# Optimization experiments

Measured on AMD Instinct MI355X. Metric: run time of the kernel, lower is better.

Reference implementation:

```python
import jax, jax.numpy as jnp
import numpy as np

B, S, D, H, BS, L, FF, V = 2, 4096, 1024, 16, 64, 4, 4096, 50000
HD = D // H; NB = S // BS; NM = NB - 2; R = 3

def layernorm(x, g, b):
    mu = x.mean(-1, keepdims=True)
    var = ((x - mu) ** 2).mean(-1, keepdims=True)
    return (x - mu) * jax.lax.rsqrt(var + 1e-5) * g + b

def bigbird_attn(x, neg, rand_attn, Wq, bq, Wk, bk, Wv, bv, Wo, bo):
    heads = lambda t: t.reshape(B, S, H, HD).transpose(0, 2, 1, 3)
    q, k, v = heads(x @ Wq + bq), heads(x @ Wk + bk), heads(x @ Wv + bv)
    scale = np.float32(1.0 / np.sqrt(HD))
    qb = q.reshape(B, H, NB, BS, HD); kb = k.reshape(B, H, NB, BS, HD); vb = v.reshape(B, H, NB, BS, HD)
    negb = neg.reshape(B, NB, BS)
    # global query blocks (first & last) attend densely to all keys
    qg = jnp.concatenate([qb[:, :, 0], qb[:, :, -1]], axis=2)  # [B,H,2*BS,HD]
    sg = jnp.einsum('bhqd,bhkd->bhqk', qg, k) * scale + neg[:, None, None, :]
    ctx_g = jnp.einsum('bhqk,bhkd->bhqd', jax.nn.softmax(sg, -1), v)
    # middle query blocks: sliding window(3) + global(2) + random(R) key blocks
    win_k = jnp.stack([kb[:, :, i:i + NM] for i in range(3)], axis=3)  # [B,H,NM,3,BS,HD]
    win_v = jnp.stack([vb[:, :, i:i + NM] for i in range(3)], axis=3)
    gidx = jnp.array([0, NB - 1])
    g_k = jnp.broadcast_to(kb[:, :, gidx][:, :, None], (B, H, NM, 2, BS, HD))
    g_v = jnp.broadcast_to(vb[:, :, gidx][:, :, None], (B, H, NM, 2, BS, HD))
    hix = jnp.arange(H)[:, None, None]
    r_k = kb[:, hix, rand_attn]  # [B,H,NM,R,BS,HD]
    r_v = vb[:, hix, rand_attn]
    K = 3 + 2 + R
    keys = jnp.concatenate([win_k, g_k, r_k], axis=3).reshape(B, H, NM, K * BS, HD)
    vals = jnp.concatenate([win_v, g_v, r_v], axis=3).reshape(B, H, NM, K * BS, HD)
    win_m = jnp.stack([negb[:, i:i + NM] for i in range(3)], axis=2)  # [B,NM,3,BS]
    g_m = jnp.broadcast_to(negb[:, gidx][:, None], (B, NM, 2, BS))
    m_wg = jnp.concatenate([win_m, g_m], axis=2).reshape(B, 1, NM, 5 * BS)
    r_m = negb[:, rand_attn].reshape(B, H, NM, R * BS)
    m_all = jnp.concatenate([jnp.broadcast_to(m_wg, (B, H, NM, 5 * BS)), r_m], axis=-1)
    sm = jnp.einsum('bhnqd,bhnkd->bhnqk', qb[:, :, 1:-1], keys) * scale + m_all[:, :, :, None, :]
    ctx_m = jnp.einsum('bhnqk,bhnkd->bhnqd', jax.nn.softmax(sm, -1), vals)
    ctx = jnp.concatenate([ctx_g[:, :, None, :BS], ctx_m, ctx_g[:, :, None, BS:]], axis=2)
    out = ctx.reshape(B, H, S, HD).transpose(0, 2, 1, 3).reshape(B, S, D)
    return out @ Wo + bo

def reference(input_ids, attention_mask, rand_attn, emb, Wq, bq, Wk, bk, Wv, bv, Wo, bo, ln1_g, ln1_b, W1, b1, W2, b2, ln2_g, ln2_b, lnf_g, lnf_b, projW, projb):
    x = emb[input_ids]
    neg = (1.0 - attention_mask.astype(jnp.float32)) * (-1e9)
    for l in range(L):  # pre-norm transformer encoder layers
        x = x + bigbird_attn(layernorm(x, ln1_g[l], ln1_b[l]), neg, rand_attn,
                             Wq[l], bq[l], Wk[l], bk[l], Wv[l], bv[l], Wo[l], bo[l])
        h = layernorm(x, ln2_g[l], ln2_b[l])
        x = x + (jax.nn.gelu(h @ W1[l] + b1[l]) @ W2[l] + b2[l])
    x = layernorm(x, lnf_g, lnf_b)
    feats = x.mean(axis=1)  # pooled output (mean over tokens)
    feats = feats / jnp.maximum(jnp.linalg.norm(feats, axis=-1, keepdims=True), 1e-12)
    return feats @ projW + projb

def setup_inputs():
    key = jax.random.key(0)
    ks = jax.random.split(key, 16)
    init = lambda k, shp: (0.02 * jax.random.normal(k, shp)).astype(jnp.float32)
    return {
        'input_ids': jax.random.randint(ks[0], (B, S), 0, V),
        'attention_mask': jnp.ones((B, S), dtype=jnp.int32),
        'rand_attn': jax.random.randint(ks[1], (H, NM, R), 1, NB - 1),
        'emb': init(ks[2], (V, D)),
        'Wq': init(ks[3], (L, D, D)), 'bq': jnp.zeros((L, D), jnp.float32),
        'Wk': init(ks[4], (L, D, D)), 'bk': jnp.zeros((L, D), jnp.float32),
        'Wv': init(ks[5], (L, D, D)), 'bv': jnp.zeros((L, D), jnp.float32),
        'Wo': init(ks[6], (L, D, D)), 'bo': jnp.zeros((L, D), jnp.float32),
        'ln1_g': jnp.ones((L, D), jnp.float32), 'ln1_b': jnp.zeros((L, D), jnp.float32),
        'W1': init(ks[7], (L, D, FF)), 'b1': jnp.zeros((L, FF), jnp.float32),
        'W2': init(ks[8], (L, FF, D)), 'b2': jnp.zeros((L, D), jnp.float32),
        'ln2_g': jnp.ones((L, D), jnp.float32), 'ln2_b': jnp.zeros((L, D), jnp.float32),
        'lnf_g': jnp.ones((D,), jnp.float32), 'lnf_b': jnp.zeros((D,), jnp.float32),
        'projW': init(ks[9], (D, 512)), 'projb': jnp.zeros((512,), jnp.float32),
    }
```

## Files before the change

### kernel.cpp

```cpp
#include <hip/hip_runtime.h>
#include <hip/hip_bf16.h>
#include <cstdint>
#include <cstddef>

#define BATCH 2
#define SEQ   4096
#define DIM   1024
#define NHEAD 16
#define HDIM  64
#define NBLK  64
#define NMID  62
#define NRAND 3
#define NLAYER 4
#define FFDIM 4096
#define ROWS  (BATCH*SEQ)
#define KSPL  8

using f32x4 = __attribute__((ext_vector_type(4))) float;
using s16x8 = __attribute__((ext_vector_type(8))) short;
using s16x4 = __attribute__((ext_vector_type(4))) short;

__device__ inline float bf2f(short s) {
    unsigned u = ((unsigned)(unsigned short)s) << 16;
    union { unsigned u; float f; } cv; cv.u = u; return cv.f;
}
__device__ inline short f2bf(float f) {
    union { float f; unsigned u; } cv; cv.f = f;
    unsigned u = cv.u;
    unsigned r = (u + 0x7fffu + ((u >> 16) & 1u)) >> 16;
    return (short)r;
}
__device__ inline float gelu_f(float x) {
    float u = 0.7978845608028654f * (x + 0.044715f * x * x * x);
    return 0.5f * x * (1.f + tanhf(u));
}

__global__ __launch_bounds__(256) void embed_kernel(
    const int* __restrict__ ids, const float* __restrict__ emb, float* __restrict__ x)
{
    int row = blockIdx.x;
    int id  = ids[row];
    ((float4*)x)[(size_t)row * 256 + threadIdx.x] =
        ((const float4*)emb)[(size_t)id * 256 + threadIdx.x];
}

__global__ __launch_bounds__(256) void neg_kernel(
    const int* __restrict__ mask, float* __restrict__ neg)
{
    int i = blockIdx.x * 256 + threadIdx.x;
    if (i < ROWS) neg[i] = (1.f - (float)mask[i]) * -1e9f;
}

template<int OUTBF>
__global__ __launch_bounds__(256) void ln_kernel(
    const float* __restrict__ x, const float* __restrict__ g,
    const float* __restrict__ bia, void* __restrict__ out)
{
    __shared__ float s1[4], s2[4];
    int row = blockIdx.x, t = threadIdx.x;
    const float* xr = x + (size_t)row * DIM;
    float4 v = ((const float4*)xr)[t];
    float s = v.x + v.y + v.z + v.w;
    #pragma unroll
    for (int o = 32; o > 0; o >>= 1) s += __shfl_xor(s, o, 64);
    if ((t & 63) == 0) s1[t >> 6] = s;
    __syncthreads();
    float mu = (s1[0] + s1[1] + s1[2] + s1[3]) * (1.f / DIM);
    float dx = v.x - mu, dy = v.y - mu, dz = v.z - mu, dw = v.w - mu;
    float q = dx*dx + dy*dy + dz*dz + dw*dw;
    #pragma unroll
    for (int o = 32; o > 0; o >>= 1) q += __shfl_xor(q, o, 64);
    if ((t & 63) == 0) s2[t >> 6] = q;
    __syncthreads();
    float var = (s2[0] + s2[1] + s2[2] + s2[3]) * (1.f / DIM);
    float rs  = rsqrtf(var + 1e-5f);
    float4 gg = ((const float4*)g)[t];
    float4 bb = ((const float4*)bia)[t];
    float o0 = dx * rs * gg.x + bb.x;
    float o1 = dy * rs * gg.y + bb.y;
    float o2 = dz * rs * gg.z + bb.z;
    float o3 = dw * rs * gg.w + bb.w;
    if (OUTBF) {
        s16x4 ov = { f2bf(o0), f2bf(o1), f2bf(o2), f2bf(o3) };
        ((s16x4*)out)[(size_t)row * (DIM/4) + t] = ov;
    } else {
        float4 ov = { o0, o1, o2, o3 };
        ((float4*)out)[(size_t)row * (DIM/4) + t] = ov;
    }
}

__global__ __launch_bounds__(256) void wconv_kernel(
    const float* __restrict__ W, short* __restrict__ Wt, int K, int N)
{
    __shared__ float tile[32][33];
    int k0 = blockIdx.x * 32, n0 = blockIdx.y * 32;
    int t = threadIdx.x;
    int r = t >> 3, c = (t & 7) * 4;
    float4 v = *(const float4*)(W + (size_t)(k0 + r) * N + n0 + c);
    tile[r][c+0] = v.x; tile[r][c+1] = v.y; tile[r][c+2] = v.z; tile[r][c+3] = v.w;
    __syncthreads();
    s16x4 ov;
    #pragma unroll
    for (int jj = 0; jj < 4; ++jj) ov[jj] = f2bf(tile[c + jj][r]);
    *(s16x4*)(Wt + (size_t)(n0 + r) * K + k0 + c) = ov;
}

__global__ __launch_bounds__(256) void vtrans_kernel(
    const short* __restrict__ vbuf, short* __restrict__ vT)
{
    __shared__ short tile[64][66];
    const int sb = blockIdx.x, h = blockIdx.y, b = blockIdx.z;
    const int t = threadIdx.x;
    {
        int row = t >> 2, c0 = (t & 3) * 16;
        const short* src = vbuf + (size_t)(b * SEQ + sb * 64 + row) * DIM + h * HDIM + c0;
        s16x8 a0 = ((const s16x8*)src)[0];
        s16x8 a1 = ((const s16x8*)src)[1];
        #pragma unroll
        for (int i = 0; i < 8; ++i) { tile[row][c0 + i] = a0[i]; tile[row][c0 + 8 + i] = a1[i]; }
    }
    __syncthreads();
    {
        int d = t >> 2, k0 = (t & 3) * 16;
        s16x8 o0, o1;
        #pragma unroll
        for (int i = 0; i < 8; ++i) { o0[i] = tile[k0 + i][d]; o1[i] = tile[k0 + 8 + i][d]; }
        short* dst = vT + (size_t)((b * NHEAD + h) * HDIM + d) * SEQ + sb * 64 + k0;
        ((s16x8*)dst)[0] = o0;
        ((s16x8*)dst)[1] = o1;
    }
}

template<int EPI>
__global__ __launch_bounds__(256) void gemm_kernel(
    const short* __restrict__ A, const short* __restrict__ Bt,
    const float* __restrict__ bias, const float* __restrict__ resid,
    void* __restrict__ Cout, int M, int N, int K)
{
    __shared__ short As[128 * 64];
    __shared__ short Bs[128 * 64];
    const int t = threadIdx.x;
    const int m0 = blockIdx.x * 128, n0 = blockIdx.y * 128;
    const int lane = t & 63, wave = t >> 6;
    const int wr = (wave >> 1) * 64, wc = (wave & 1) * 64;
    const int srow = t >> 3;
    const int scolb = (t & 7) * 16;

    f32x4 acc[4][4];
    #pragma unroll
    for (int m = 0; m < 4; ++m)
        #pragma unroll
        for (int n = 0; n < 4; ++n)
            acc[m][n] = f32x4{0.f, 0.f, 0.f, 0.f};

    const short* Arow = A  + (size_t)(m0 + srow) * K + (scolb >> 1);
    const short* Brow = Bt + (size_t)(n0 + srow) * K + (scolb >> 1);

    for (int kt = 0; kt < K; kt += 64) {
        s16x8 ra[4], rb[4];
        #pragma unroll
        for (int p = 0; p < 4; ++p) {
            ra[p] = *(const s16x8*)(Arow + (size_t)(p * 32) * K + kt);
            rb[p] = *(const s16x8*)(Brow + (size_t)(p * 32) * K + kt);
        }
        __syncthreads();
        #pragma unroll
        for (int p = 0; p < 4; ++p) {
            int row = p * 32 + srow;
            int boff = row * 128 + (scolb ^ ((row & 7) << 4));
            *(s16x8*)((char*)As + boff) = ra[p];
            *(s16x8*)((char*)Bs + boff) = rb[p];
        }
        __syncthreads();
        #pragma unroll
        for (int kk = 0; kk < 2; ++kk) {
            s16x8 af[4], bfr[4];
            #pragma unroll
            for (int i = 0; i < 4; ++i) {
                int cb = kk * 64 + ((lane >> 4) << 4);
                int r  = wr + i * 16 + (lane & 15);
                af[i]  = *(const s16x8*)((const char*)As + r * 128 + (cb ^ ((r & 7) << 4)));
                int r2 = wc + i * 16 + (lane & 15);
                bfr[i] = *(const s16x8*)((const char*)Bs + r2 * 128 + (cb ^ ((r2 & 7) << 4)));
            }
            #pragma unroll
            for (int m = 0; m < 4; ++m)
                #pragma unroll
                for (int n = 0; n < 4; ++n)
                    acc[m][n] = __builtin_amdgcn_mfma_f32_16x16x32_bf16(
                        af[m], bfr[n], acc[m][n], 0, 0, 0);
        }
    }

    const int rbase = m0 + wr + ((lane >> 4) << 2);
    const int cbase = n0 + wc + (lane & 15);
    #pragma unroll
    for (int m = 0; m < 4; ++m) {
        #pragma unroll
        for (int n = 0; n < 4; ++n) {
            #pragma unroll
            for (int j = 0; j < 4; ++j) {
                int row = rbase + m * 16 + j;
                int col = cbase + n * 16;
                float val = acc[m][n][j] + bias[col];
                size_t idx = (size_t)row * N + col;
                if (EPI == 1) val = gelu_f(val);
                if (EPI == 2) ((float*)Cout)[idx] = val + resid[idx];
                else          ((short*)Cout)[idx] = f2bf(val);
            }
        }
    }
}


__device__ inline void attn_tile_mfma(
    const short* __restrict__ kglob,
    const short* __restrict__ vtglob,
    const float* __restrict__ negp,
    short* Ks, short* Vs, float* kmask,
    const s16x8* qfrag, f32x4* o, float& mr, float& lsum)
{
    const int t = threadIdx.x;
    const int lane = t & 63;
    const int q15 = lane & 15, g = lane >> 4;
    const int sw = (lane & 7) << 4;

    {
        int row = t >> 2, c0 = (t & 3) * 16;
        int rsw = (row & 7) << 4;
        const short* ksrc = kglob + (size_t)row * DIM + c0;
        s16x8 a0 = ((const s16x8*)ksrc)[0];
        s16x8 a1 = ((const s16x8*)ksrc)[1];
        char* kdst = (char*)Ks + row * 128;
        *(s16x8*)(kdst + ((c0 * 2)      ^ rsw)) = a0;
        *(s16x8*)(kdst + ((c0 * 2 + 16) ^ rsw)) = a1;
        const short* vsrc = vtglob + (size_t)row * SEQ + c0;
        s16x8 b0 = ((const s16x8*)vsrc)[0];
        s16x8 b1 = ((const s16x8*)vsrc)[1];
        char* vdst = (char*)Vs + row * 128;
        *(s16x8*)(vdst + ((c0 * 2)      ^ rsw)) = b0;
        *(s16x8*)(vdst + ((c0 * 2 + 16) ^ rsw)) = b1;
        if (t < 16) ((float4*)kmask)[t] = ((const float4*)negp)[t];
    }
    __syncthreads();

    f32x4 s[4];
    #pragma unroll
    for (int f = 0; f < 4; ++f) s[f] = f32x4{0.f, 0.f, 0.f, 0.f};
    #pragma unroll
    for (int ch = 0; ch < 2; ++ch) {
        #pragma unroll
        for (int f = 0; f < 4; ++f) {
            s16x8 kf = *(const s16x8*)((const char*)Ks + (16 * f + q15) * 128 + ((ch * 64 + g * 16) ^ sw));
            s[f] = __builtin_amdgcn_mfma_f32_16x16x32_bf16(kf, qfrag[ch], s[f], 0, 0, 0);
        }
    }

    float p[4][4];
    float mt = -1e30f;
    #pragma unroll
    for (int f = 0; f < 4; ++f) {
        float4 km = ((const float4*)kmask)[f * 4 + g];
        #pragma unroll
        for (int j = 0; j < 4; ++j) {
            float val = s[f][j] * 0.125f + ((const float*)&km)[j];
            p[f][j] = val;
            mt = fmaxf(mt, val);
        }
    }
    mt = fmaxf(mt, __shfl_xor(mt, 16, 64));
    mt = fmaxf(mt, __shfl_xor(mt, 32, 64));
    float mn = fmaxf(mr, mt);
    float psum = 0.f;
    #pragma unroll
    for (int f = 0; f < 4; ++f)
        #pragma unroll
        for (int j = 0; j < 4; ++j) {
            float e = __expf(p[f][j] - mn);
            p[f][j] = e;
            psum += e;
        }
    psum += __shfl_xor(psum, 16, 64);
    psum += __shfl_xor(psum, 32, 64);
    float fc = __expf(mr - mn);
    mr = mn;
    lsum = lsum * fc + psum;
    #pragma unroll
    for (int dt = 0; dt < 4; ++dt)
        #pragma unroll
        for (int j = 0; j < 4; ++j) o[dt][j] *= fc;

    unsigned pk[4][2];
    #pragma unroll
    for (int f = 0; f < 4; ++f)
        #pragma unroll
        for (int pp = 0; pp < 2; ++pp)
            pk[f][pp] = ((unsigned)(unsigned short)f2bf(p[f][2 * pp + 1]) << 16)
                      |  (unsigned)(unsigned short)f2bf(p[f][2 * pp]);

    const int bsel = (lane >> 4) & 1, asel = (lane >> 5) & 1;
    #pragma unroll
    for (int c = 0; c < 2; ++c) {
        union { s16x8 v; int u[4]; } pb;
        #pragma unroll
        for (int w = 0; w < 4; ++w) {
            int src = q15 + 16 * (2 * bsel + (w >> 1));
            int lo = __shfl((int)pk[2 * c][w & 1], src, 64);
            int hi = __shfl((int)pk[2 * c + 1][w & 1], src, 64);
            pb.u[w] = asel ? hi : lo;
        }
        #pragma unroll
        for (int dt = 0; dt < 4; ++dt) {
            s16x8 vf = *(const s16x8*)((const char*)Vs + (16 * dt + q15) * 128 + ((c * 64 + g * 16) ^ sw));
            o[dt] = __builtin_amdgcn_mfma_f32_16x16x32_bf16(vf, pb.v, o[dt], 0, 0, 0);
        }
    }
    __syncthreads();
}

__device__ inline void stage_q64_swz(const short* __restrict__ qglob, short* Qs)
{
    int t = threadIdx.x;
    int row = t >> 2, c0 = (t & 3) * 16;
    int rsw = (row & 7) << 4;
    const short* src = qglob + (size_t)row * DIM + c0;
    s16x8 a0 = ((const s16x8*)src)[0];
    s16x8 a1 = ((const s16x8*)src)[1];
    char* dst = (char*)Qs + row * 128;
    *(s16x8*)(dst + ((c0 * 2)      ^ rsw)) = a0;
    *(s16x8*)(dst + ((c0 * 2 + 16) ^ rsw)) = a1;
}

__global__ __launch_bounds__(256) void attn_middle_mfma(
    const short* __restrict__ q, const short* __restrict__ k, const short* __restrict__ vT,
    const float* __restrict__ neg, const int* __restrict__ rand_attn, short* __restrict__ ctx)
{
    __shared__ short Qs[64 * 64];
    __shared__ short Ks[64 * 64];
    __shared__ short Vs[64 * 64];
    __shared__ float kmask[64];

    const int j = blockIdx.x, h = blockIdx.y, b = blockIdx.z;
    const int n = j + 1;
    const int t = threadIdx.x;
    const int lane = t & 63, wave = t >> 6;
    const int q15 = lane & 15, g = lane >> 4;
    const int sw = (lane & 7) << 4;

    stage_q64_swz(q + (size_t)(b * SEQ + n * 64) * DIM + h * HDIM, Qs);
    __syncthreads();

    s16x8 qfrag[2];
    {
        int qrow = wave * 16 + q15;
        #pragma unroll
        for (int ch = 0; ch < 2; ++ch)
            qfrag[ch] = *(const s16x8*)((const char*)Qs + qrow * 128 + ((ch * 64 + g * 16) ^ sw));
    }

    int kbl[8];
    kbl[0] = n - 1; kbl[1] = n; kbl[2] = n + 1; kbl[3] = 0; kbl[4] = NBLK - 1;
    {
        const int* ra = rand_attn + ((size_t)h * NMID + j) * NRAND;
        kbl[5] = ra[0]; kbl[6] = ra[1]; kbl[7] = ra[2];
    }

    f32x4 o[4];
    #pragma unroll
    for (int dt = 0; dt < 4; ++dt) o[dt] = f32x4{0.f, 0.f, 0.f, 0.f};
    float mr = -1e30f, lsum = 0.f;

    const short* kbase  = k  + (size_t)b * SEQ * DIM + h * HDIM;
    const short* vtbase = vT + (size_t)(b * NHEAD + h) * HDIM * SEQ;
    const float* negb   = neg + (size_t)b * SEQ;

    #pragma unroll 1
    for (int ib = 0; ib < 8; ++ib) {
        int kbn = kbl[ib];
        attn_tile_mfma(kbase + (size_t)kbn * 64 * DIM, vtbase + kbn * 64,
                       negb + kbn * 64, Ks, Vs, kmask, qfrag, o, mr, lsum);
    }

    float inv = 1.f / lsum;
    short* obase = ctx + (size_t)(b * SEQ + n * 64 + wave * 16 + q15) * DIM + h * HDIM;
    #pragma unroll
    for (int dt = 0; dt < 4; ++dt) {
        s16x4 ov;
        #pragma unroll
        for (int jj = 0; jj < 4; ++jj) ov[jj] = f2bf(o[dt][jj] * inv);
        *(s16x4*)(obase + dt * 16 + g * 4) = ov;
    }
}

__global__ __launch_bounds__(256) void attn_global_mfma(
    const short* __restrict__ q, const short* __restrict__ k, const short* __restrict__ vT,
    const float* __restrict__ neg, float* __restrict__ part)
{
    __shared__ short Qs[64 * 64];
    __shared__ short Ks[64 * 64];
    __shared__ short Vs[64 * 64];
    __shared__ float kmask[64];

    const int qb = blockIdx.x >> 3, ks = blockIdx.x & 7;
    const int h = blockIdx.y, b = blockIdx.z;
    const int tok0 = qb ? (SEQ - 64) : 0;
    const int t = threadIdx.x;
    const int lane = t & 63, wave = t >> 6;
    const int q15 = lane & 15, g = lane >> 4;
    const int sw = (lane & 7) << 4;

    stage_q64_swz(q + (size_t)(b * SEQ + tok0) * DIM + h * HDIM, Qs);
    __syncthreads();

    s16x8 qfrag[2];
    {
        int qrow = wave * 16 + q15;
        #pragma unroll
        for (int ch = 0; ch < 2; ++ch)
            qfrag[ch] = *(const s16x8*)((const char*)Qs + qrow * 128 + ((ch * 64 + g * 16) ^ sw));
    }

    f32x4 o[4];
    #pragma unroll
    for (int dt = 0; dt < 4; ++dt) o[dt] = f32x4{0.f, 0.f, 0.f, 0.f};
    float mr = -1e30f, lsum = 0.f;

    const short* kbase  = k  + (size_t)b * SEQ * DIM + h * HDIM;
    const short* vtbase = vT + (size_t)(b * NHEAD + h) * HDIM * SEQ;
    const float* negb   = neg + (size_t)b * SEQ;

    #pragma unroll 1
    for (int ib = 0; ib < 8; ++ib) {
        int kbn = ks * 8 + ib;
        attn_tile_mfma(kbase + (size_t)kbn * 64 * DIM, vtbase + kbn * 64,
                       negb + kbn * 64, Ks, Vs, kmask, qfrag, o, mr, lsum);
    }

    float* pbase = part + ((size_t)(((b * NHEAD + h) * 2 + qb) * KSPL + ks)) * 4224;
    int qrow = wave * 16 + q15;
    #pragma unroll
    for (int dt = 0; dt < 4; ++dt)
        *(f32x4*)(pbase + qrow * 64 + dt * 16 + g * 4) = o[dt];
    if (g == 0) { pbase[4096 + qrow] = mr; pbase[4160 + qrow] = lsum; }
}

__global__ __launch_bounds__(256) void attn_greduce(
    const float* __restrict__ part, short* __restrict__ ctx)
{
    const int qb = blockIdx.x, h = blockIdx.y, b = blockIdx.z;
    const int tok0 = qb ? (SEQ - 64) : 0;
    const int t = threadIdx.x;
    const int qq = t >> 2, d0 = (t & 3) * 16;
    const float* base = part + ((size_t)(((b * NHEAD + h) * 2 + qb) * KSPL)) * 4224;

    float m = -1e30f;
    #pragma unroll 1
    for (int s = 0; s < KSPL; ++s)
        m = fmaxf(m, base[(size_t)s * 4224 + 4096 + qq]);
    float L = 0.f;
    float acc[16];
    #pragma unroll
    for (int i = 0; i < 16; ++i) acc[i] = 0.f;
    #pragma unroll 1
    for (int s = 0; s < KSPL; ++s) {
        const float* bp = base + (size_t)s * 4224;
        float w = __expf(bp[4096 + qq] - m);
        L += w * bp[4160 + qq];
        const float4* row = (const float4*)(bp + qq * 64 + d0);
        #pragma unroll
        for (int v4 = 0; v4 < 4; ++v4) {
            float4 val = row[v4];
            acc[v4 * 4 + 0] = fmaf(w, val.x, acc[v4 * 4 + 0]);
            acc[v4 * 4 + 1] = fmaf(w, val.y, acc[v4 * 4 + 1]);
            acc[v4 * 4 + 2] = fmaf(w, val.z, acc[v4 * 4 + 2]);
            acc[v4 * 4 + 3] = fmaf(w, val.w, acc[v4 * 4 + 3]);
        }
    }
    float inv = 1.f / L;
    short* dst = ctx + (size_t)(b * SEQ + tok0 + qq) * DIM + h * HDIM + d0;
    s16x8 o0, o1;
    #pragma unroll
    for (int i = 0; i < 8; ++i) { o0[i] = f2bf(acc[i] * inv); o1[i] = f2bf(acc[8 + i] * inv); }
    ((s16x8*)dst)[0] = o0;
    ((s16x8*)dst)[1] = o1;
}

__global__ __launch_bounds__(256) void colmean_kernel(
    const float* __restrict__ xln, float* __restrict__ feats)
{
    __shared__ float red[8][33];
    int c = blockIdx.x, b = blockIdx.y;
    int dd = threadIdx.x & 31, rg = threadIdx.x >> 5;
    const float* base = xln + (size_t)b * SEQ * DIM + c * 32 + dd;
    float s = 0.f;
    for (int rr = rg; rr < SEQ; rr += 8) s += base[(size_t)rr * DIM];
    red[rg][dd] = s;
    __syncthreads();
    if (rg == 0) {
        float tot = s;
        #pragma unroll
        for (int i = 1; i < 8; ++i) tot += red[i][dd];
        feats[b * DIM + c * 32 + dd] = tot * (1.f / SEQ);
    }
}

__global__ __launch_bounds__(256) void head_kernel(
    const float* __restrict__ feats, const float* __restrict__ projW,
    const float* __restrict__ projb, float* __restrict__ out)
{
    __shared__ float f[DIM];
    __shared__ float slots[4];
    int b = blockIdx.x, t = threadIdx.x;
    float ss = 0.f;
    for (int i = t; i < DIM; i += 256) {
        float vv = feats[b * DIM + i];
        f[i] = vv;
        ss += vv * vv;
    }
    #pragma unroll
    for (int o = 32; o > 0; o >>= 1) ss += __shfl_xor(ss, o, 64);
    if ((t & 63) == 0) slots[t >> 6] = ss;
    __syncthreads();
    float nrm = sqrtf(slots[0] + slots[1] + slots[2] + slots[3]);
    float inv = 1.f / fmaxf(nrm, 1e-12f);
    for (int o = t; o < 512; o += 256) {
        float acc = 0.f;
        for (int d = 0; d < DIM; ++d)
            acc = fmaf(f[d], projW[(size_t)d * 512 + o], acc);
        out[b * 512 + o] = acc * inv + projb[o];
    }
}

extern "C" void kernel_launch(void* const* d_in, const int* in_sizes, int n_in,
                              void* d_out, int out_size, void* d_ws, size_t ws_size,
                              hipStream_t stream)
{
    (void)in_sizes; (void)n_in; (void)out_size; (void)ws_size;
    const int*   ids   = (const int*)d_in[0];
    const int*   amask = (const int*)d_in[1];
    const int*   rnd   = (const int*)d_in[2];
    const float* emb   = (const float*)d_in[3];
    const float* Wq    = (const float*)d_in[4];
    const float* bq    = (const float*)d_in[5];
    const float* Wk    = (const float*)d_in[6];
    const float* bk    = (const float*)d_in[7];
    const float* Wv    = (const float*)d_in[8];
    const float* bv    = (const float*)d_in[9];
    const float* Wo    = (const float*)d_in[10];
    const float* bo    = (const float*)d_in[11];
    const float* ln1g  = (const float*)d_in[12];
    const float* ln1b  = (const float*)d_in[13];
    const float* W1    = (const float*)d_in[14];
    const float* b1    = (const float*)d_in[15];
    const float* W2    = (const float*)d_in[16];
    const float* b2    = (const float*)d_in[17];
    const float* ln2g  = (const float*)d_in[18];
    const float* ln2b  = (const float*)d_in[19];
    const float* lnfg  = (const float*)d_in[20];
    const float* lnfb  = (const float*)d_in[21];
    const float* projW = (const float*)d_in[22];
    const float* projb = (const float*)d_in[23];
    float* out = (float*)d_out;

    char* ws = (char*)d_ws;
    size_t off = 0;
    float* x    = (float*)(ws + off); off += (size_t)ROWS * DIM * 4;
    float* xn_f = (float*)(ws + off);
    short* xn_b = (short*)(ws + off); off += (size_t)ROWS * DIM * 4;
    short* qb   = (short*)(ws + off); off += (size_t)ROWS * DIM * 2;
    short* kbuf = (short*)(ws + off); off += (size_t)ROWS * DIM * 2;
    short* vbuf = (short*)(ws + off); off += (size_t)ROWS * DIM * 2;
    short* vT   = (short*)(ws + off); off += (size_t)ROWS * DIM * 2;
    short* ctxb = (short*)(ws + off); off += (size_t)ROWS * DIM * 2;
    short* ffb  = (short*)(ws + off); off += (size_t)ROWS * FFDIM * 2;
    short* wt   = (short*)(ws + off); off += (size_t)FFDIM * DIM * 2;
    float* neg  = (float*)(ws + off); off += (size_t)ROWS * 4;
    float* feats= (float*)(ws + off); off += (size_t)BATCH * DIM * 4;
    float* part = (float*)(ws + off); off += (size_t)BATCH * NHEAD * 2 * KSPL * 4224 * 4;

    embed_kernel<<<ROWS, 256, 0, stream>>>(ids, emb, x);
    neg_kernel<<<(ROWS + 255) / 256, 256, 0, stream>>>(amask, neg);

    for (int l = 0; l < NLAYER; ++l) {
        ln_kernel<1><<<ROWS, 256, 0, stream>>>(x, ln1g + l * DIM, ln1b + l * DIM, xn_b);

        wconv_kernel<<<dim3(DIM/32, DIM/32), 256, 0, stream>>>(Wq + (size_t)l*DIM*DIM, wt, DIM, DIM);
        gemm_kernel<0><<<dim3(ROWS/128, DIM/128), 256, 0, stream>>>(xn_b, wt, bq + l*DIM, nullptr, qb,   ROWS, DIM, DIM);
        wconv_kernel<<<dim3(DIM/32, DIM/32), 256, 0, stream>>>(Wk + (size_t)l*DIM*DIM, wt, DIM, DIM);
        gemm_kernel<0><<<dim3(ROWS/128, DIM/128), 256, 0, stream>>>(xn_b, wt, bk + l*DIM, nullptr, kbuf, ROWS, DIM, DIM);
        wconv_kernel<<<dim3(DIM/32, DIM/32), 256, 0, stream>>>(Wv + (size_t)l*DIM*DIM, wt, DIM, DIM);
        gemm_kernel<0><<<dim3(ROWS/128, DIM/128), 256, 0, stream>>>(xn_b, wt, bv + l*DIM, nullptr, vbuf, ROWS, DIM, DIM);

        vtrans_kernel<<<dim3(SEQ/64, NHEAD, BATCH), 256, 0, stream>>>(vbuf, vT);

        attn_global_mfma<<<dim3(2 * KSPL, NHEAD, BATCH), 256, 0, stream>>>(qb, kbuf, vT, neg, part);
        attn_middle_mfma<<<dim3(NMID, NHEAD, BATCH), 256, 0, stream>>>(qb, kbuf, vT, neg, rnd, ctxb);
        attn_greduce<<<dim3(2, NHEAD, BATCH), 256, 0, stream>>>(part, ctxb);

        wconv_kernel<<<dim3(DIM/32, DIM/32), 256, 0, stream>>>(Wo + (size_t)l*DIM*DIM, wt, DIM, DIM);
        gemm_kernel<2><<<dim3(ROWS/128, DIM/128), 256, 0, stream>>>(ctxb, wt, bo + l*DIM, x, x, ROWS, DIM, DIM);

        ln_kernel<1><<<ROWS, 256, 0, stream>>>(x, ln2g + l * DIM, ln2b + l * DIM, xn_b);

        wconv_kernel<<<dim3(DIM/32, FFDIM/32), 256, 0, stream>>>(W1 + (size_t)l*DIM*FFDIM, wt, DIM, FFDIM);
        gemm_kernel<1><<<dim3(ROWS/128, FFDIM/128), 256, 0, stream>>>(xn_b, wt, b1 + l*FFDIM, nullptr, ffb, ROWS, FFDIM, DIM);
        wconv_kernel<<<dim3(FFDIM/32, DIM/32), 256, 0, stream>>>(W2 + (size_t)l*FFDIM*DIM, wt, FFDIM, DIM);
        gemm_kernel<2><<<dim3(ROWS/128, DIM/128), 256, 0, stream>>>(ffb, wt, b2 + l*DIM, x, x, ROWS, DIM, FFDIM);
    }

    ln_kernel<0><<<ROWS, 256, 0, stream>>>(x, lnfg, lnfb, xn_f);
    colmean_kernel<<<dim3(32, BATCH), 256, 0, stream>>>(xn_f, feats);
    head_kernel<<<BATCH, 256, 0, stream>>>(feats, projW, projb, out);
}
```

Baseline: 1.972 ms.

## Fuse QKV GEMMs, use direct global-to-LDS loads, parallelize column mean

The Q, K and V projections now share one concatenated weight and bias and run as a single GEMM into an interleaved qkv buffer, and the attention kernels read it with a 3*DIM stride. The GEMM mainloop stages tiles with global_load_lds (16-byte direct-to-LDS loads), dropping the register round trip and the XOR swizzle, and adds a trailing barrier. The final column mean becomes a two-stage reduction over many more blocks. Risks: without the swizzle, LDS reads may hit bank conflicts, and the GEMM still has no double buffering.

```diff
diff --git a/kernel.cpp b/kernel.cpp
--- a/kernel.cpp
+++ b/kernel.cpp
@@ -15,6 +15,7 @@
 #define FFDIM 4096
 #define ROWS  (BATCH*SEQ)
 #define KSPL  8
+#define QKVLD (3*DIM)
 
 using f32x4 = __attribute__((ext_vector_type(4))) float;
 using s16x8 = __attribute__((ext_vector_type(8))) short;
@@ -35,6 +36,13 @@
     return 0.5f * x * (1.f + tanhf(u));
 }
 
+__device__ inline void gload16(const short* g, short* l) {
+    __builtin_amdgcn_global_load_lds(
+        (const __attribute__((address_space(1))) void*)g,
+        (__attribute__((address_space(3))) void*)l,
+        16, 0, 0);
+}
+
 __global__ __launch_bounds__(256) void embed_kernel(
     const int* __restrict__ ids, const float* __restrict__ emb, float* __restrict__ x)
 {
@@ -49,6 +57,15 @@
 {
     int i = blockIdx.x * 256 + threadIdx.x;
     if (i < ROWS) neg[i] = (1.f - (float)mask[i]) * -1e9f;
+}
+
+__global__ __launch_bounds__(256) void biaspack_kernel(
+    const float* __restrict__ bq, const float* __restrict__ bk,
+    const float* __restrict__ bv, float* __restrict__ b3)
+{
+    int i = blockIdx.x * 256 + threadIdx.x;
+    float v = (i < DIM) ? bq[i] : (i < 2 * DIM) ? bk[i - DIM] : bv[i - 2 * DIM];
+    b3[i] = v;
 }
 
 template<int OUTBF>
@@ -106,14 +123,14 @@
 }
 
 __global__ __launch_bounds__(256) void vtrans_kernel(
-    const short* __restrict__ vbuf, short* __restrict__ vT)
+    const short* __restrict__ qkv, short* __restrict__ vT)
 {
     __shared__ short tile[64][66];
     const int sb = blockIdx.x, h = blockIdx.y, b = blockIdx.z;
     const int t = threadIdx.x;
     {
         int row = t >> 2, c0 = (t & 3) * 16;
-        const short* src = vbuf + (size_t)(b * SEQ + sb * 64 + row) * DIM + h * HDIM + c0;
+        const short* src = qkv + 2 * DIM + (size_t)(b * SEQ + sb * 64 + row) * QKVLD + h * HDIM + c0;
         s16x8 a0 = ((const s16x8*)src)[0];
         s16x8 a1 = ((const s16x8*)src)[1];
         #pragma unroll
@@ -143,8 +160,8 @@
     const int m0 = blockIdx.x * 128, n0 = blockIdx.y * 128;
     const int lane = t & 63, wave = t >> 6;
     const int wr = (wave >> 1) * 64, wc = (wave & 1) * 64;
-    const int srow = t >> 3;
-    const int scolb = (t & 7) * 16;
+    const int lrow = lane >> 3;
+    const int lk   = (lane & 7) * 8;
 
     f32x4 acc[4][4];
     #pragma unroll
@@ -153,23 +170,13 @@
         for (int n = 0; n < 4; ++n)
             acc[m][n] = f32x4{0.f, 0.f, 0.f, 0.f};
 
-    const short* Arow = A  + (size_t)(m0 + srow) * K + (scolb >> 1);
-    const short* Brow = Bt + (size_t)(n0 + srow) * K + (scolb >> 1);
-
     for (int kt = 0; kt < K; kt += 64) {
-        s16x8 ra[4], rb[4];
-        #pragma unroll
-        for (int p = 0; p < 4; ++p) {
-            ra[p] = *(const s16x8*)(Arow + (size_t)(p * 32) * K + kt);
-            rb[p] = *(const s16x8*)(Brow + (size_t)(p * 32) * K + kt);
-        }
-        __syncthreads();
-        #pragma unroll
-        for (int p = 0; p < 4; ++p) {
-            int row = p * 32 + srow;
-            int boff = row * 128 + (scolb ^ ((row & 7) << 4));
-            *(s16x8*)((char*)As + boff) = ra[p];
-            *(s16x8*)((char*)Bs + boff) = rb[p];
+        #pragma unroll
+        for (int c = 0; c < 4; ++c) {
+            int chunk = wave * 4 + c;
+            int row = chunk * 8 + lrow;
+            gload16(A  + (size_t)(m0 + row) * K + kt + lk, As + chunk * 512);
+            gload16(Bt + (size_t)(n0 + row) * K + kt + lk, Bs + chunk * 512);
         }
         __syncthreads();
         #pragma unroll
@@ -177,11 +184,10 @@
             s16x8 af[4], bfr[4];
             #pragma unroll
             for (int i = 0; i < 4; ++i) {
-                int cb = kk * 64 + ((lane >> 4) << 4);
-                int r  = wr + i * 16 + (lane & 15);
-                af[i]  = *(const s16x8*)((const char*)As + r * 128 + (cb ^ ((r & 7) << 4)));
-                int r2 = wc + i * 16 + (lane & 15);
-                bfr[i] = *(const s16x8*)((const char*)Bs + r2 * 128 + (cb ^ ((r2 & 7) << 4)));
+                int rA = wr + i * 16 + (lane & 15);
+                af[i]  = *(const s16x8*)(As + rA * 64 + kk * 32 + (lane >> 4) * 8);
+                int rB = wc + i * 16 + (lane & 15);
+                bfr[i] = *(const s16x8*)(Bs + rB * 64 + kk * 32 + (lane >> 4) * 8);
             }
             #pragma unroll
             for (int m = 0; m < 4; ++m)
@@ -190,6 +196,7 @@
                     acc[m][n] = __builtin_amdgcn_mfma_f32_16x16x32_bf16(
                         af[m], bfr[n], acc[m][n], 0, 0, 0);
         }
+        __syncthreads();
     }
 
     const int rbase = m0 + wr + ((lane >> 4) << 2);
@@ -217,6 +224,7 @@
     const short* __restrict__ kglob,
     const short* __restrict__ vtglob,
     const float* __restrict__ negp,
+    int kld,
     short* Ks, short* Vs, float* kmask,
     const s16x8* qfrag, f32x4* o, float& mr, float& lsum)
 {
@@ -228,7 +236,7 @@
     {
         int row = t >> 2, c0 = (t & 3) * 16;
         int rsw = (row & 7) << 4;
-        const short* ksrc = kglob + (size_t)row * DIM + c0;
+        const short* ksrc = kglob + (size_t)row * kld + c0;
         s16x8 a0 = ((const s16x8*)ksrc)[0];
         s16x8 a1 = ((const s16x8*)ksrc)[1];
         char* kdst = (char*)Ks + row * 128;
@@ -318,12 +326,12 @@
     __syncthreads();
 }
 
-__device__ inline void stage_q64_swz(const short* __restrict__ qglob, short* Qs)
+__device__ inline void stage_q64_swz(const short* __restrict__ qglob, int qld, short* Qs)
 {
     int t = threadIdx.x;
     int row = t >> 2, c0 = (t & 3) * 16;
     int rsw = (row & 7) << 4;
-    const short* src = qglob + (size_t)row * DIM + c0;
+    const short* src = qglob + (size_t)row * qld + c0;
     s16x8 a0 = ((const s16x8*)src)[0];
     s16x8 a1 = ((const s16x8*)src)[1];
     char* dst = (char*)Qs + row * 128;
@@ -332,7 +340,7 @@
 }
 
 __global__ __launch_bounds__(256) void attn_middle_mfma(
-    const short* __restrict__ q, const short* __restrict__ k, const short* __restrict__ vT,
+    const short* __restrict__ qkv, const short* __restrict__ vT,
     const float* __restrict__ neg, const int* __restrict__ rand_attn, short* __restrict__ ctx)
 {
     __shared__ short Qs[64 * 64];
@@ -347,7 +355,7 @@
     const int q15 = lane & 15, g = lane >> 4;
     const int sw = (lane & 7) << 4;
 
-    stage_q64_swz(q + (size_t)(b * SEQ + n * 64) * DIM + h * HDIM, Qs);
+    stage_q64_swz(qkv + (size_t)(b * SEQ + n * 64) * QKVLD + h * HDIM, QKVLD, Qs);
     __syncthreads();
 
     s16x8 qfrag[2];
@@ -370,15 +378,15 @@
     for (int dt = 0; dt < 4; ++dt) o[dt] = f32x4{0.f, 0.f, 0.f, 0.f};
     float mr = -1e30f, lsum = 0.f;
 
-    const short* kbase  = k  + (size_t)b * SEQ * DIM + h * HDIM;
+    const short* kbase  = qkv + DIM + (size_t)b * SEQ * QKVLD + h * HDIM;
     const short* vtbase = vT + (size_t)(b * NHEAD + h) * HDIM * SEQ;
     const float* negb   = neg + (size_t)b * SEQ;
 
     #pragma unroll 1
     for (int ib = 0; ib < 8; ++ib) {
         int kbn = kbl[ib];
-        attn_tile_mfma(kbase + (size_t)kbn * 64 * DIM, vtbase + kbn * 64,
-                       negb + kbn * 64, Ks, Vs, kmask, qfrag, o, mr, lsum);
+        attn_tile_mfma(kbase + (size_t)kbn * 64 * QKVLD, vtbase + kbn * 64,
+                       negb + kbn * 64, QKVLD, Ks, Vs, kmask, qfrag, o, mr, lsum);
     }
 
     float inv = 1.f / lsum;
@@ -393,7 +401,7 @@
 }
 
 __global__ __launch_bounds__(256) void attn_global_mfma(
-    const short* __restrict__ q, const short* __restrict__ k, const short* __restrict__ vT,
+    const short* __restrict__ qkv, const short* __restrict__ vT,
     const float* __restrict__ neg, float* __restrict__ part)
 {
     __shared__ short Qs[64 * 64];
@@ -409,7 +417,7 @@
     const int q15 = lane & 15, g = lane >> 4;
     const int sw = (lane & 7) << 4;
 
-    stage_q64_swz(q + (size_t)(b * SEQ + tok0) * DIM + h * HDIM, Qs);
+    stage_q64_swz(qkv + (size_t)(b * SEQ + tok0) * QKVLD + h * HDIM, QKVLD, Qs);
     __syncthreads();
 
     s16x8 qfrag[2];
@@ -425,15 +433,15 @@
     for (int dt = 0; dt < 4; ++dt) o[dt] = f32x4{0.f, 0.f, 0.f, 0.f};
     float mr = -1e30f, lsum = 0.f;
 
-    const short* kbase  = k  + (size_t)b * SEQ * DIM + h * HDIM;
+    const short* kbase  = qkv + DIM + (size_t)b * SEQ * QKVLD + h * HDIM;
     const short* vtbase = vT + (size_t)(b * NHEAD + h) * HDIM * SEQ;
     const float* negb   = neg + (size_t)b * SEQ;
 
     #pragma unroll 1
     for (int ib = 0; ib < 8; ++ib) {
         int kbn = ks * 8 + ib;
-        attn_tile_mfma(kbase + (size_t)kbn * 64 * DIM, vtbase + kbn * 64,
-                       negb + kbn * 64, Ks, Vs, kmask, qfrag, o, mr, lsum);
+        attn_tile_mfma(kbase + (size_t)kbn * 64 * QKVLD, vtbase + kbn * 64,
+                       negb + kbn * 64, QKVLD, Ks, Vs, kmask, qfrag, o, mr, lsum);
     }
 
     float* pbase = part + ((size_t)(((b * NHEAD + h) * 2 + qb) * KSPL + ks)) * 4224;
@@ -485,23 +493,33 @@
     ((s16x8*)dst)[1] = o1;
 }
 
-__global__ __launch_bounds__(256) void colmean_kernel(
-    const float* __restrict__ xln, float* __restrict__ feats)
-{
-    __shared__ float red[8][33];
-    int c = blockIdx.x, b = blockIdx.y;
-    int dd = threadIdx.x & 31, rg = threadIdx.x >> 5;
-    const float* base = xln + (size_t)b * SEQ * DIM + c * 32 + dd;
-    float s = 0.f;
-    for (int rr = rg; rr < SEQ; rr += 8) s += base[(size_t)rr * DIM];
-    red[rg][dd] = s;
-    __syncthreads();
-    if (rg == 0) {
-        float tot = s;
-        #pragma unroll
-        for (int i = 1; i < 8; ++i) tot += red[i][dd];
-        feats[b * DIM + c * 32 + dd] = tot * (1.f / SEQ);
-    }
+__global__ __launch_bounds__(256) void colsum1_kernel(
+    const float* __restrict__ xln, float* __restrict__ partial)
+{
+    const int ch = blockIdx.x, b = blockIdx.y, t = threadIdx.x;
+    const float* base = xln + ((size_t)b * SEQ + ch * 32) * DIM + t * 4;
+    float4 acc = {0.f, 0.f, 0.f, 0.f};
+    #pragma unroll 4
+    for (int r = 0; r < 32; ++r) {
+        float4 v = *(const float4*)(base + (size_t)r * DIM);
+        acc.x += v.x; acc.y += v.y; acc.z += v.z; acc.w += v.w;
+    }
+    *(float4*)(partial + ((size_t)(b * 128 + ch)) * DIM + t * 4) = acc;
+}
+
+__global__ __launch_bounds__(256) void colsum2_kernel(
+    const float* __restrict__ partial, float* __restrict__ feats)
+{
+    const int b = blockIdx.x, t = threadIdx.x;
+    float4 acc = {0.f, 0.f, 0.f, 0.f};
+    #pragma unroll 1
+    for (int ch = 0; ch < 128; ++ch) {
+        float4 v = *(const float4*)(partial + ((size_t)(b * 128 + ch)) * DIM + t * 4);
+        acc.x += v.x; acc.y += v.y; acc.z += v.z; acc.w += v.w;
+    }
+    const float is = 1.f / SEQ;
+    float4 o = { acc.x * is, acc.y * is, acc.z * is, acc.w * is };
+    *(float4*)(feats + (size_t)b * DIM + t * 4) = o;
 }
 
 __global__ __launch_bounds__(256) void head_kernel(
@@ -567,16 +585,16 @@
     float* x    = (float*)(ws + off); off += (size_t)ROWS * DIM * 4;
     float* xn_f = (float*)(ws + off);
     short* xn_b = (short*)(ws + off); off += (size_t)ROWS * DIM * 4;
-    short* qb   = (short*)(ws + off); off += (size_t)ROWS * DIM * 2;
-    short* kbuf = (short*)(ws + off); off += (size_t)ROWS * DIM * 2;
-    short* vbuf = (short*)(ws + off); off += (size_t)ROWS * DIM * 2;
+    short* qkv  = (short*)(ws + off); off += (size_t)ROWS * QKVLD * 2;
     short* vT   = (short*)(ws + off); off += (size_t)ROWS * DIM * 2;
     short* ctxb = (short*)(ws + off); off += (size_t)ROWS * DIM * 2;
     short* ffb  = (short*)(ws + off); off += (size_t)ROWS * FFDIM * 2;
     short* wt   = (short*)(ws + off); off += (size_t)FFDIM * DIM * 2;
     float* neg  = (float*)(ws + off); off += (size_t)ROWS * 4;
+    float* bias3= (float*)(ws + off); off += (size_t)QKVLD * 4;
     float* feats= (float*)(ws + off); off += (size_t)BATCH * DIM * 4;
     float* part = (float*)(ws + off); off += (size_t)BATCH * NHEAD * 2 * KSPL * 4224 * 4;
+    float* cpart= (float*)(ws + off); off += (size_t)BATCH * 128 * DIM * 4;
 
     embed_kernel<<<ROWS, 256, 0, stream>>>(ids, emb, x);
     neg_kernel<<<(ROWS + 255) / 256, 256, 0, stream>>>(amask, neg);
@@ -584,17 +602,16 @@
     for (int l = 0; l < NLAYER; ++l) {
         ln_kernel<1><<<ROWS, 256, 0, stream>>>(x, ln1g + l * DIM, ln1b + l * DIM, xn_b);
 
-        wconv_kernel<<<dim3(DIM/32, DIM/32), 256, 0, stream>>>(Wq + (size_t)l*DIM*DIM, wt, DIM, DIM);
-        gemm_kernel<0><<<dim3(ROWS/128, DIM/128), 256, 0, stream>>>(xn_b, wt, bq + l*DIM, nullptr, qb,   ROWS, DIM, DIM);
-        wconv_kernel<<<dim3(DIM/32, DIM/32), 256, 0, stream>>>(Wk + (size_t)l*DIM*DIM, wt, DIM, DIM);
-        gemm_kernel<0><<<dim3(ROWS/128, DIM/128), 256, 0, stream>>>(xn_b, wt, bk + l*DIM, nullptr, kbuf, ROWS, DIM, DIM);
-        wconv_kernel<<<dim3(DIM/32, DIM/32), 256, 0, stream>>>(Wv + (size_t)l*DIM*DIM, wt, DIM, DIM);
-        gemm_kernel<0><<<dim3(ROWS/128, DIM/128), 256, 0, stream>>>(xn_b, wt, bv + l*DIM, nullptr, vbuf, ROWS, DIM, DIM);
-
-        vtrans_kernel<<<dim3(SEQ/64, NHEAD, BATCH), 256, 0, stream>>>(vbuf, vT);
-
-        attn_global_mfma<<<dim3(2 * KSPL, NHEAD, BATCH), 256, 0, stream>>>(qb, kbuf, vT, neg, part);
-        attn_middle_mfma<<<dim3(NMID, NHEAD, BATCH), 256, 0, stream>>>(qb, kbuf, vT, neg, rnd, ctxb);
+        wconv_kernel<<<dim3(DIM/32, DIM/32), 256, 0, stream>>>(Wq + (size_t)l*DIM*DIM, wt,                 DIM, DIM);
+        wconv_kernel<<<dim3(DIM/32, DIM/32), 256, 0, stream>>>(Wk + (size_t)l*DIM*DIM, wt + 1024*1024,     DIM, DIM);
+        wconv_kernel<<<dim3(DIM/32, DIM/32), 256, 0, stream>>>(Wv + (size_t)l*DIM*DIM, wt + 2*1024*1024,   DIM, DIM);
+        biaspack_kernel<<<QKVLD/256, 256, 0, stream>>>(bq + l*DIM, bk + l*DIM, bv + l*DIM, bias3);
+        gemm_kernel<0><<<dim3(ROWS/128, QKVLD/128), 256, 0, stream>>>(xn_b, wt, bias3, nullptr, qkv, ROWS, QKVLD, DIM);
+
+        vtrans_kernel<<<dim3(SEQ/64, NHEAD, BATCH), 256, 0, stream>>>(qkv, vT);
+
+        attn_global_mfma<<<dim3(2 * KSPL, NHEAD, BATCH), 256, 0, stream>>>(qkv, vT, neg, part);
+        attn_middle_mfma<<<dim3(NMID, NHEAD, BATCH), 256, 0, stream>>>(qkv, vT, neg, rnd, ctxb);
         attn_greduce<<<dim3(2, NHEAD, BATCH), 256, 0, stream>>>(part, ctxb);
 
         wconv_kernel<<<dim3(DIM/32, DIM/32), 256, 0, stream>>>(Wo + (size_t)l*DIM*DIM, wt, DIM, DIM);
@@ -609,6 +626,7 @@
     }
 
     ln_kernel<0><<<ROWS, 256, 0, stream>>>(x, lnfg, lnfb, xn_f);
-    colmean_kernel<<<dim3(32, BATCH), 256, 0, stream>>>(xn_f, feats);
+    colsum1_kernel<<<dim3(SEQ/32, BATCH), 256, 0, stream>>>(xn_f, cpart);
+    colsum2_kernel<<<BATCH, 256, 0, stream>>>(cpart, feats);
     head_kernel<<<BATCH, 256, 0, stream>>>(feats, projW, projb, out);
 }
```

Measured after the change: 2.037 ms. 3.3% more time.
